# Optimization experiments

Measured on AMD Instinct MI355X. Metric: run time of the kernel, lower is better.

## Reference

```python
import jax, jax.numpy as jnp
import numpy as np

HIDDEN = 1024
NUM_EXPERTS = 8
TOP_K = 2
INNER = HIDDEN * 2
B, S = 4, 2048


def setup_inputs() -> dict:
    key = jax.random.key(0)
    ks = jax.random.split(key, 8)
    sd = 1.0 / np.sqrt(HIDDEN)
    si = 1.0 / np.sqrt(INNER)
    return {
        "x": jax.random.normal(ks[0], (B, S, HIDDEN), dtype=jnp.float32),
        "Wr": jax.random.uniform(ks[1], (HIDDEN, NUM_EXPERTS), jnp.float32, -sd, sd),
        "br": jax.random.uniform(ks[2], (NUM_EXPERTS,), jnp.float32, -sd, sd),
        "W1": jax.random.uniform(ks[3], (NUM_EXPERTS, HIDDEN, INNER), jnp.float32, -sd, sd),
        "b1": jax.random.uniform(ks[4], (NUM_EXPERTS, INNER), jnp.float32, -sd, sd),
        "W2": jax.random.uniform(ks[5], (NUM_EXPERTS, INNER, HIDDEN), jnp.float32, -si, si),
        "b2": jax.random.uniform(ks[6], (NUM_EXPERTS, HIDDEN), jnp.float32, -si, si),
    }


def reference(x, Wr, br, W1, b1, W2, b2):
    batch, seq, hidden = x.shape
    tokens = x.reshape(-1, hidden)                       # [N, d]
    n = tokens.shape[0]
    logits = tokens @ Wr + br                            # [N, E]
    top_w, top_i = jax.lax.top_k(logits, TOP_K)          # [N, k]
    top_w = jax.nn.softmax(top_w, axis=-1)
    # Dense per-token expert weights (zero outside top-k) — equivalent to the
    # sorted-dispatch + index_add combine in the original.
    weights = jnp.zeros((n, NUM_EXPERTS), dtype=top_w.dtype)
    weights = weights.at[jnp.arange(n)[:, None], top_i].add(top_w)  # [N, E]
    out = jnp.zeros_like(tokens)
    for e in range(NUM_EXPERTS):  # fixed small loop over experts
        h = jax.nn.relu(tokens @ W1[e] + b1[e])          # [N, inner]
        y = h @ W2[e] + b2[e]                            # [N, d]
        out = out + y * weights[:, e:e + 1]
    return out.reshape(batch, seq, hidden)
```

## Files before the change

### kernel.cpp

```cpp
#include <hip/hip_runtime.h>
#include <stdint.h>

#define HID    1024
#define EXPERTS 8
#define TOPK   2
#define INNER  2048
#define NTOK   8192
#define NPAIR  (NTOK * TOPK)
#define MAXT   136
#define BM 128
#define BN 256
#define BK 64
#define NSLOT 304
#define AFFS  24

typedef _Float16 f16;
typedef f16   f16x8 __attribute__((ext_vector_type(8)));
typedef float f32x4 __attribute__((ext_vector_type(4)));

#define VMCNT(n) asm volatile("s_waitcnt vmcnt(" #n ")" ::: "memory")
#define BARRIER() do { __builtin_amdgcn_s_barrier(); asm volatile("" ::: "memory"); } while (0)

__device__ __forceinline__ void gload_lds16(const void* g, void* l) {
  __builtin_amdgcn_global_load_lds(
      (const __attribute__((address_space(1))) void*)g,
      (__attribute__((address_space(3))) void*)l, 16, 0, 0);
}

__global__ void router_kernel(const float* __restrict__ x,
                              const float* __restrict__ Wr,
                              const float* __restrict__ br,
                              int* __restrict__ e_sel, float* __restrict__ w_sel) {
  int gid  = blockIdx.x * blockDim.x + threadIdx.x;
  int wid  = gid >> 6;
  int lane = gid & 63;
  if (wid >= NTOK) return;

  const f32x4* xr = (const f32x4*)(x + (size_t)wid * HID);
  float acc[EXPERTS];
#pragma unroll
  for (int e = 0; e < EXPERTS; ++e) acc[e] = 0.f;
#pragma unroll
  for (int j = 0; j < HID / 256; ++j) {
    f32x4 xv = xr[j * 64 + lane];
    int   k  = (j * 64 + lane) * 4;
    const float* wr = Wr + (size_t)k * EXPERTS;
#pragma unroll
    for (int r = 0; r < 4; ++r) {
      float xs = xv[r];
      f32x4 w0 = *(const f32x4*)(wr + r * 8);
      f32x4 w1 = *(const f32x4*)(wr + r * 8 + 4);
#pragma unroll
      for (int e = 0; e < 4; ++e) { acc[e] += xs * w0[e]; acc[4 + e] += xs * w1[e]; }
    }
  }
#pragma unroll
  for (int e = 0; e < EXPERTS; ++e) {
#pragma unroll
    for (int off = 32; off > 0; off >>= 1) acc[e] += __shfl_xor(acc[e], off);
  }
  if (lane == 0) {
    float lg[EXPERTS];
#pragma unroll
    for (int e = 0; e < EXPERTS; ++e) lg[e] = acc[e] + br[e];
    int e0 = 0; float l0 = lg[0];
#pragma unroll
    for (int e = 1; e < EXPERTS; ++e) if (lg[e] > l0) { l0 = lg[e]; e0 = e; }
    int e1 = -1; float l1 = -3.4e38f;
#pragma unroll
    for (int e = 0; e < EXPERTS; ++e) if (e != e0 && lg[e] > l1) { l1 = lg[e]; e1 = e; }
    float a  = __expf(l1 - l0);
    float w0 = 1.f / (1.f + a);
    float w1 = a * w0;
    e_sel[wid * 2]     = e0;  e_sel[wid * 2 + 1] = e1;
    w_sel[wid * 2]     = w0;  w_sel[wid * 2 + 1] = w1;
  }
}

__global__ __launch_bounds__(1024) void dispatch_kernel(
    const int* __restrict__ e_sel, const float* __restrict__ w_sel,
    int* __restrict__ tok_list, float* __restrict__ wt_list,
    int* __restrict__ counts, int* __restrict__ bases,
    int* __restrict__ slot_e, int* __restrict__ slot_m0,
    int* __restrict__ slot_g, int* __restrict__ tinfo) {
  __shared__ int scnt[EXPERTS][1024];
  __shared__ int etot[EXPERTS];
  __shared__ int ebase[EXPERTS];
  int tid = threadIdx.x, lane = tid & 63, wv = tid >> 6;

  int myE[16]; float myW[16];
  int lc[EXPERTS];
#pragma unroll
  for (int e = 0; e < EXPERTS; ++e) lc[e] = 0;
#pragma unroll
  for (int i = 0; i < 16; ++i) {
    int p = tid * 16 + i;
    myE[i] = e_sel[p];
    myW[i] = w_sel[p];
#pragma unroll
    for (int e = 0; e < EXPERTS; ++e) lc[e] += (myE[i] == e);
  }
#pragma unroll
  for (int e = 0; e < EXPERTS; ++e) scnt[e][tid] = lc[e];
  __syncthreads();

  if (wv < EXPERTS) {
    int run = 0;
    for (int c = 0; c < 16; ++c) {
      int v = scnt[wv][c * 64 + lane];
      int incl = v;
#pragma unroll
      for (int off = 1; off < 64; off <<= 1) {
        int n = __shfl_up(incl, off);
        if (lane >= off) incl += n;
      }
      scnt[wv][c * 64 + lane] = run + incl - v;
      run += __shfl(incl, 63);
    }
    if (lane == 0) etot[wv] = run;
  }
  __syncthreads();

  if (tid < NSLOT) slot_e[tid] = -1;
  __syncthreads();
  if (tid == 0) {
    int s = 0;
    for (int e = 0; e < EXPERTS; ++e) {
      ebase[e] = s; bases[e] = s; counts[e] = etot[e]; s += etot[e];
    }
    int ov = AFFS * EXPERTS, gt = 0;
    for (int e = 0; e < EXPERTS; ++e) {
      int ntl = (etot[e] + BM - 1) / BM;
      for (int i = 0; i < ntl; ++i) {
        int sl = (i < AFFS) ? (e + EXPERTS * i) : (ov++);
        slot_e[sl] = e; slot_m0[sl] = i * BM; slot_g[sl] = gt++;
      }
    }
    tinfo[0] = gt;
  }
  __syncthreads();

  int cur[EXPERTS];
#pragma unroll
  for (int e = 0; e < EXPERTS; ++e) cur[e] = ebase[e] + scnt[e][tid];
#pragma unroll
  for (int i = 0; i < 16; ++i) {
    int p = 0;
#pragma unroll
    for (int e = 0; e < EXPERTS; ++e) if (myE[i] == e) p = cur[e]++;
    tok_list[p] = (tid * 16 + i) >> 1;
    wt_list[p]  = myW[i];
  }
}

__global__ void convert_x_kernel(const float* __restrict__ x,
                                 f16* __restrict__ x16, int n8) {
  int i = blockIdx.x * blockDim.x + threadIdx.x;
  int stride = gridDim.x * blockDim.x;
  for (; i < n8; i += stride) {
    f32x4 a = ((const f32x4*)x)[i * 2];
    f32x4 b = ((const f32x4*)x)[i * 2 + 1];
    f16x8 o;
#pragma unroll
    for (int j = 0; j < 4; ++j) { o[j] = (f16)a[j]; o[4 + j] = (f16)b[j]; }
    ((f16x8*)x16)[i] = o;
  }
}

__global__ void transpose_cvt_kernel(const float* __restrict__ src,
                                     f16* __restrict__ dst, int R, int C) {
  __shared__ float tile[32][33];
  int z = blockIdx.z;
  src += (size_t)z * R * C;
  dst += (size_t)z * R * C;
  int c0 = blockIdx.x * 32, r0 = blockIdx.y * 32;
  int tx = threadIdx.x, ty = threadIdx.y;
#pragma unroll
  for (int i = 0; i < 4; ++i)
    tile[ty + i * 8][tx] = src[(size_t)(r0 + ty + i * 8) * C + c0 + tx];
  __syncthreads();
#pragma unroll
  for (int i = 0; i < 4; ++i)
    dst[(size_t)(c0 + ty + i * 8) * R + r0 + tx] = (f16)tile[tx][ty + i * 8];
}


#define STAGE6(BUF) do {                                                      \
  _Pragma("unroll") for (int i_ = 0; i_ < 2; ++i_) {                          \
    gload_lds16(gA[i_], (BUF) + i_ * 4096 + wid * 512); gA[i_] += BK;         \
  }                                                                           \
  _Pragma("unroll") for (int i_ = 0; i_ < 4; ++i_) {                          \
    gload_lds16(gB[i_], (BUF) + 8192 + i_ * 4096 + wid * 512); gB[i_] += BK;  \
  }                                                                           \
} while (0)

#define COMPUTE16(BUF) do {                                                   \
  _Pragma("unroll") for (int kk_ = 0; kk_ < 2; ++kk_) {                       \
    int lc_ = (kk_ * 4 + hi) ^ sa;                                            \
    f16x8 af_[4], bf_[4];                                                     \
    _Pragma("unroll") for (int mi_ = 0; mi_ < 4; ++mi_)                       \
      af_[mi_] = *(const f16x8*)((BUF) + (wm + mi_ * 16 + ar) * 64 + lc_ * 8);\
    _Pragma("unroll") for (int ni_ = 0; ni_ < 4; ++ni_)                       \
      bf_[ni_] = *(const f16x8*)((BUF) + 8192 +                               \
                                 (wn + ni_ * 16 + ar) * 64 + lc_ * 8);        \
    _Pragma("unroll") for (int mi_ = 0; mi_ < 4; ++mi_)                       \
      _Pragma("unroll") for (int ni_ = 0; ni_ < 4; ++ni_)                     \
        acc[mi_][ni_] = __builtin_amdgcn_mfma_f32_16x16x32_f16(               \
            af_[mi_], bf_[ni_], acc[mi_][ni_], 0, 0, 0);                      \
  }                                                                           \
} while (0)

#define PIPELINE_LOOP(NT) do {                                                \
  STAGE6(q0); STAGE6(q1);                                                     \
  VMCNT(6); BARRIER();                                                        \
  for (int t = 0; t < (NT); ++t) {                                            \
    if (t + 2 < (NT)) { STAGE6(q2); }                                         \
    COMPUTE16(q0);                                                            \
    if (t + 2 < (NT)) { VMCNT(6); } else { VMCNT(0); }                        \
    BARRIER();                                                                \
    f16* tm_ = q0; q0 = q1; q1 = q2; q2 = tm_;                                \
  }                                                                           \
} while (0)

__global__ __launch_bounds__(512, 2) void gemm1_kernel(
    const f16* __restrict__ x16, const f16* __restrict__ w1t,
    const float* __restrict__ bias1, const int* __restrict__ tok_list,
    const int* __restrict__ counts, const int* __restrict__ bases,
    const int* __restrict__ slot_e, const int* __restrict__ slot_m0,
    const int* __restrict__ slot_g, int c0, int G,
    f16* __restrict__ h16) {
  int sx = blockIdx.x;
  int e  = slot_e[sx];
  if (e < 0) return;
  int g  = slot_g[sx];
  if (g < c0 || g >= c0 + G) return;
  int m0 = slot_m0[sx];
  int cnt = counts[e], base = bases[e];
  int n0 = blockIdx.y * BN;
  const f16* Bg = w1t + (size_t)e * INNER * HID;

  __shared__ __align__(16) f16 LDS[3 * 24576];
  f16 *q0 = LDS, *q1 = LDS + 24576, *q2 = LDS + 2 * 24576;

  int tid = threadIdx.x, lane = tid & 63, wid = tid >> 6;
  int wm = (wid >> 2) * 64, wn = (wid & 3) * 64;
  int ar = lane & 15, hi = lane >> 4, sa = ar & 7;

  int trow = tid >> 3;
  int gcol = (tid & 7) ^ (trow & 7);
  const f16* gA[2];
  const f16* gB[4];
#pragma unroll
  for (int i = 0; i < 2; ++i) {
    int row = i * 64 + trow;
    int tok = tok_list[base + min(m0 + row, cnt - 1)];
    gA[i] = x16 + (size_t)tok * HID + gcol * 8;
  }
#pragma unroll
  for (int i = 0; i < 4; ++i) {
    int row = i * 64 + trow;
    gB[i] = Bg + (size_t)(n0 + row) * HID + gcol * 8;
  }

  f32x4 acc[4][4];
#pragma unroll
  for (int i = 0; i < 4; ++i)
#pragma unroll
    for (int j = 0; j < 4; ++j) acc[i][j] = (f32x4){0.f, 0.f, 0.f, 0.f};

  PIPELINE_LOOP(HID / BK);

  int colc = ar, rbase = hi * 4;
  float bb[4];
#pragma unroll
  for (int ni = 0; ni < 4; ++ni)
    bb[ni] = bias1[(size_t)e * INNER + n0 + wn + ni * 16 + colc];
#pragma unroll
  for (int mi = 0; mi < 4; ++mi)
#pragma unroll
    for (int r = 0; r < 4; ++r) {
      int ml = wm + mi * 16 + rbase + r;
      if (m0 + ml < cnt) {
        size_t rowoff = (size_t)((g - c0) * BM + ml) * INNER + n0 + wn + colc;
#pragma unroll
        for (int ni = 0; ni < 4; ++ni) {
          float v = acc[mi][ni][r] + bb[ni];
          h16[rowoff + ni * 16] = (f16)fmaxf(v, 0.f);
        }
      }
    }
}

__global__ __launch_bounds__(512, 2) void gemm2_kernel(
    const f16* __restrict__ h16, const f16* __restrict__ w2t,
    const float* __restrict__ bias2, const int* __restrict__ tok_list,
    const float* __restrict__ wt_list, const int* __restrict__ counts,
    const int* __restrict__ bases,
    const int* __restrict__ slot_e, const int* __restrict__ slot_m0,
    const int* __restrict__ slot_g, int c0, int G,
    float* __restrict__ out) {
  int sx = blockIdx.x;
  int e  = slot_e[sx];
  if (e < 0) return;
  int g  = slot_g[sx];
  if (g < c0 || g >= c0 + G) return;
  int m0 = slot_m0[sx];
  int cnt = counts[e], base = bases[e];
  int d0 = blockIdx.y * BN;
  int kc = blockIdx.z;
  int koff = kc * (INNER / 2);
  const f16* Bg = w2t + (size_t)e * HID * INNER;

  __shared__ __align__(16) f16 LDS[3 * 24576];
  f16 *q0 = LDS, *q1 = LDS + 24576, *q2 = LDS + 2 * 24576;

  int tid = threadIdx.x, lane = tid & 63, wid = tid >> 6;
  int wm = (wid >> 2) * 64, wn = (wid & 3) * 64;
  int ar = lane & 15, hi = lane >> 4, sa = ar & 7;

  int trow = tid >> 3;
  int gcol = (tid & 7) ^ (trow & 7);
  const f16* gA[2];
  const f16* gB[4];
#pragma unroll
  for (int i = 0; i < 2; ++i) {
    int row  = i * 64 + trow;
    int lrow = min(m0 + row, cnt - 1) - m0;
    gA[i] = h16 + ((size_t)(g - c0) * BM + lrow) * INNER + koff + gcol * 8;
  }
#pragma unroll
  for (int i = 0; i < 4; ++i) {
    int row = i * 64 + trow;
    gB[i] = Bg + (size_t)(d0 + row) * INNER + koff + gcol * 8;
  }

  f32x4 acc[4][4];
#pragma unroll
  for (int i = 0; i < 4; ++i)
#pragma unroll
    for (int j = 0; j < 4; ++j) acc[i][j] = (f32x4){0.f, 0.f, 0.f, 0.f};

  PIPELINE_LOOP((INNER / 2) / BK);

  int colc = ar, rbase = hi * 4;
  float bb[4];
#pragma unroll
  for (int ni = 0; ni < 4; ++ni)
    bb[ni] = (kc == 0) ? bias2[(size_t)e * HID + d0 + wn + ni * 16 + colc] : 0.f;
#pragma unroll
  for (int mi = 0; mi < 4; ++mi)
#pragma unroll
    for (int r = 0; r < 4; ++r) {
      int ml = wm + mi * 16 + rbase + r;
      if (m0 + ml < cnt) {
        int   p   = base + m0 + ml;
        int   tok = tok_list[p];
        float w   = wt_list[p];
        float* orow = out + (size_t)tok * HID + d0 + wn + colc;
#pragma unroll
        for (int ni = 0; ni < 4; ++ni) {
          float v = acc[mi][ni][r] + bb[ni];
          atomicAdd(orow + ni * 16, v * w);
        }
      }
    }
}

extern "C" void kernel_launch(void* const* d_in, const int* in_sizes, int n_in,
                              void* d_out, int out_size, void* d_ws, size_t ws_size,
                              hipStream_t stream) {
  (void)in_sizes; (void)n_in;
  const float* x  = (const float*)d_in[0];
  const float* Wr = (const float*)d_in[1];
  const float* br = (const float*)d_in[2];
  const float* W1 = (const float*)d_in[3];
  const float* b1 = (const float*)d_in[4];
  const float* W2 = (const float*)d_in[5];
  const float* b2 = (const float*)d_in[6];
  float* out = (float*)d_out;

  char*  ws  = (char*)d_ws;
  size_t off = 0;
  auto alloc = [&](size_t bytes) {
    char* p = ws + off;
    off += bytes; off = (off + 255) & ~(size_t)255;
    return p;
  };
  int*   tok_list = (int*)alloc(NPAIR * sizeof(int));
  float* wt_list  = (float*)alloc(NPAIR * sizeof(float));
  int*   e_sel    = (int*)alloc(NTOK * 2 * sizeof(int));
  float* w_sel    = (float*)alloc(NTOK * 2 * sizeof(float));
  int*   counts   = (int*)alloc(EXPERTS * sizeof(int));
  int*   bases    = (int*)alloc(EXPERTS * sizeof(int));
  int*   slot_e   = (int*)alloc(NSLOT * sizeof(int));
  int*   slot_m0  = (int*)alloc(NSLOT * sizeof(int));
  int*   slot_g   = (int*)alloc(NSLOT * sizeof(int));
  int*   tinfo    = (int*)alloc(16 * sizeof(int));
  f16*   w1t      = (f16*)alloc((size_t)EXPERTS * HID * INNER * sizeof(f16));
  f16*   w2t      = (f16*)alloc((size_t)EXPERTS * HID * INNER * sizeof(f16));
  f16*   x16      = (f16*)alloc((size_t)NTOK * HID * sizeof(f16));
  const size_t TILE_BYTES = (size_t)BM * INNER * sizeof(f16);
  size_t rem = (ws_size > off) ? (ws_size - off) : 0;
  int G = (int)(rem / TILE_BYTES);
  if (G < 1) G = 1;
  if (G > MAXT) G = MAXT;
  int nch = (MAXT + G - 1) / G;
  f16* h16 = (f16*)(ws + off);

  hipMemsetAsync(out, 0, (size_t)out_size * sizeof(float), stream);

  convert_x_kernel<<<2048, 256, 0, stream>>>(x, x16, NTOK * HID / 8);
  transpose_cvt_kernel<<<dim3(INNER / 32, HID / 32, EXPERTS), dim3(32, 8), 0, stream>>>(
      W1, w1t, HID, INNER);
  transpose_cvt_kernel<<<dim3(HID / 32, INNER / 32, EXPERTS), dim3(32, 8), 0, stream>>>(
      W2, w2t, INNER, HID);
  router_kernel<<<NTOK / 4, 256, 0, stream>>>(x, Wr, br, e_sel, w_sel);
  dispatch_kernel<<<1, 1024, 0, stream>>>(e_sel, w_sel, tok_list, wt_list,
                                          counts, bases, slot_e, slot_m0, slot_g, tinfo);

  for (int c = 0; c < nch; ++c) {
    int c0 = c * G;
    gemm1_kernel<<<dim3(NSLOT, INNER / BN, 1), 512, 0, stream>>>(
        x16, w1t, b1, tok_list, counts, bases, slot_e, slot_m0, slot_g, c0, G, h16);
    gemm2_kernel<<<dim3(NSLOT, HID / BN, 2), 512, 0, stream>>>(
        h16, w2t, b2, tok_list, wt_list, counts, bases, slot_e, slot_m0, slot_g, c0, G, out);
  }
}
```

Baseline: 533.4 us.

## Shrink GEMM tiles to 128x128x32 with 256-thread blocks and new swizzle

Both expert GEMM kernels now use 128x128 output tiles with BK=32 and 4 waves per block instead of 128x256 tiles, BK=64 and 8 waves. The LDS staging layout and XOR swizzle are rewritten for 32-wide rows, and launch bounds and the slot/affinity constants are changed to match. The aim is a smaller LDS footprint, more resident blocks per CU and more blocks to fill the GPU. In exchange each block reuses loaded data less, and the shorter K step means more barriers per unit of work.

```diff
diff --git a/kernel.cpp b/kernel.cpp
--- a/kernel.cpp
+++ b/kernel.cpp
@@ -9,10 +9,10 @@
 #define NPAIR  (NTOK * TOPK)
 #define MAXT   136
 #define BM 128
-#define BN 256
-#define BK 64
-#define NSLOT 304
-#define AFFS  24
+#define BN 128
+#define BK 32
+#define AFFS  17
+#define NSLOT 200
 
 typedef _Float16 f16;
 typedef f16   f16x8 __attribute__((ext_vector_type(8)));
@@ -185,44 +185,39 @@
 }
 
 
-#define STAGE6(BUF) do {                                                      \
+#define STAGE4(BUF) do {                                                      \
   _Pragma("unroll") for (int i_ = 0; i_ < 2; ++i_) {                          \
-    gload_lds16(gA[i_], (BUF) + i_ * 4096 + wid * 512); gA[i_] += BK;         \
-  }                                                                           \
-  _Pragma("unroll") for (int i_ = 0; i_ < 4; ++i_) {                          \
-    gload_lds16(gB[i_], (BUF) + 8192 + i_ * 4096 + wid * 512); gB[i_] += BK;  \
+    gload_lds16(gA[i_], (BUF) + i_ * 2048 + wid * 512); gA[i_] += BK;         \
+    gload_lds16(gB[i_], (BUF) + 4096 + i_ * 2048 + wid * 512); gB[i_] += BK;  \
   }                                                                           \
 } while (0)
 
-#define COMPUTE16(BUF) do {                                                   \
-  _Pragma("unroll") for (int kk_ = 0; kk_ < 2; ++kk_) {                       \
-    int lc_ = (kk_ * 4 + hi) ^ sa;                                            \
-    f16x8 af_[4], bf_[4];                                                     \
-    _Pragma("unroll") for (int mi_ = 0; mi_ < 4; ++mi_)                       \
-      af_[mi_] = *(const f16x8*)((BUF) + (wm + mi_ * 16 + ar) * 64 + lc_ * 8);\
+#define COMPUTE8(BUF) do {                                                    \
+  f16x8 af_[4], bf_[4];                                                       \
+  _Pragma("unroll") for (int mi_ = 0; mi_ < 4; ++mi_)                         \
+    af_[mi_] = *(const f16x8*)((BUF) + (wm + mi_ * 16 + ar) * 32 + cswz * 8); \
+  _Pragma("unroll") for (int ni_ = 0; ni_ < 4; ++ni_)                         \
+    bf_[ni_] = *(const f16x8*)((BUF) + 4096 +                                 \
+                               (wn + ni_ * 16 + ar) * 32 + cswz * 8);         \
+  _Pragma("unroll") for (int mi_ = 0; mi_ < 4; ++mi_)                         \
     _Pragma("unroll") for (int ni_ = 0; ni_ < 4; ++ni_)                       \
-      bf_[ni_] = *(const f16x8*)((BUF) + 8192 +                               \
-                                 (wn + ni_ * 16 + ar) * 64 + lc_ * 8);        \
-    _Pragma("unroll") for (int mi_ = 0; mi_ < 4; ++mi_)                       \
-      _Pragma("unroll") for (int ni_ = 0; ni_ < 4; ++ni_)                     \
-        acc[mi_][ni_] = __builtin_amdgcn_mfma_f32_16x16x32_f16(               \
-            af_[mi_], bf_[ni_], acc[mi_][ni_], 0, 0, 0);                      \
-  }                                                                           \
+      acc[mi_][ni_] = __builtin_amdgcn_mfma_f32_16x16x32_f16(                 \
+          af_[mi_], bf_[ni_], acc[mi_][ni_], 0, 0, 0);                        \
 } while (0)
 
 #define PIPELINE_LOOP(NT) do {                                                \
-  STAGE6(q0); STAGE6(q1);                                                     \
-  VMCNT(6); BARRIER();                                                        \
+  STAGE4(q0); STAGE4(q1);                                                     \
+  VMCNT(4); BARRIER();                                                        \
   for (int t = 0; t < (NT); ++t) {                                            \
-    if (t + 2 < (NT)) { STAGE6(q2); }                                         \
-    COMPUTE16(q0);                                                            \
-    if (t + 2 < (NT)) { VMCNT(6); } else { VMCNT(0); }                        \
+    if (t + 2 < (NT)) { STAGE4(q2); }                                         \
+    COMPUTE8(q0);                                                             \
+    if (t + 2 < (NT)) { VMCNT(4); } else { VMCNT(0); }                        \
     BARRIER();                                                                \
     f16* tm_ = q0; q0 = q1; q1 = q2; q2 = tm_;                                \
   }                                                                           \
 } while (0)
 
-__global__ __launch_bounds__(512, 2) void gemm1_kernel(
+__global__ __launch_bounds__(256, 3) void gemm1_kernel(
     const f16* __restrict__ x16, const f16* __restrict__ w1t,
     const float* __restrict__ bias1, const int* __restrict__ tok_list,
     const int* __restrict__ counts, const int* __restrict__ bases,
@@ -239,26 +234,23 @@
   int n0 = blockIdx.y * BN;
   const f16* Bg = w1t + (size_t)e * INNER * HID;
 
-  __shared__ __align__(16) f16 LDS[3 * 24576];
-  f16 *q0 = LDS, *q1 = LDS + 24576, *q2 = LDS + 2 * 24576;
+  __shared__ __align__(16) f16 LDS[3 * 8192];
+  f16 *q0 = LDS, *q1 = LDS + 8192, *q2 = LDS + 2 * 8192;
 
   int tid = threadIdx.x, lane = tid & 63, wid = tid >> 6;
-  int wm = (wid >> 2) * 64, wn = (wid & 3) * 64;
-  int ar = lane & 15, hi = lane >> 4, sa = ar & 7;
-
-  int trow = tid >> 3;
-  int gcol = (tid & 7) ^ (trow & 7);
+  int wm = (wid >> 1) * 64, wn = (wid & 1) * 64;
+  int ar = lane & 15, hi = lane >> 4;
+  int cswz = hi ^ ((ar >> 1) & 3);
+
+  int trow = tid >> 2;
+  int gcol = (tid & 3) ^ ((tid >> 3) & 3);
   const f16* gA[2];
-  const f16* gB[4];
+  const f16* gB[2];
 #pragma unroll
   for (int i = 0; i < 2; ++i) {
     int row = i * 64 + trow;
     int tok = tok_list[base + min(m0 + row, cnt - 1)];
     gA[i] = x16 + (size_t)tok * HID + gcol * 8;
-  }
-#pragma unroll
-  for (int i = 0; i < 4; ++i) {
-    int row = i * 64 + trow;
     gB[i] = Bg + (size_t)(n0 + row) * HID + gcol * 8;
   }
 
@@ -291,7 +283,7 @@
     }
 }
 
-__global__ __launch_bounds__(512, 2) void gemm2_kernel(
+__global__ __launch_bounds__(256, 3) void gemm2_kernel(
     const f16* __restrict__ h16, const f16* __restrict__ w2t,
     const float* __restrict__ bias2, const int* __restrict__ tok_list,
     const float* __restrict__ wt_list, const int* __restrict__ counts,
@@ -311,26 +303,23 @@
   int koff = kc * (INNER / 2);
   const f16* Bg = w2t + (size_t)e * HID * INNER;
 
-  __shared__ __align__(16) f16 LDS[3 * 24576];
-  f16 *q0 = LDS, *q1 = LDS + 24576, *q2 = LDS + 2 * 24576;
+  __shared__ __align__(16) f16 LDS[3 * 8192];
+  f16 *q0 = LDS, *q1 = LDS + 8192, *q2 = LDS + 2 * 8192;
 
   int tid = threadIdx.x, lane = tid & 63, wid = tid >> 6;
-  int wm = (wid >> 2) * 64, wn = (wid & 3) * 64;
-  int ar = lane & 15, hi = lane >> 4, sa = ar & 7;
-
-  int trow = tid >> 3;
-  int gcol = (tid & 7) ^ (trow & 7);
+  int wm = (wid >> 1) * 64, wn = (wid & 1) * 64;
+  int ar = lane & 15, hi = lane >> 4;
+  int cswz = hi ^ ((ar >> 1) & 3);
+
+  int trow = tid >> 2;
+  int gcol = (tid & 3) ^ ((tid >> 3) & 3);
   const f16* gA[2];
-  const f16* gB[4];
+  const f16* gB[2];
 #pragma unroll
   for (int i = 0; i < 2; ++i) {
     int row  = i * 64 + trow;
     int lrow = min(m0 + row, cnt - 1) - m0;
     gA[i] = h16 + ((size_t)(g - c0) * BM + lrow) * INNER + koff + gcol * 8;
-  }
-#pragma unroll
-  for (int i = 0; i < 4; ++i) {
-    int row = i * 64 + trow;
     gB[i] = Bg + (size_t)(d0 + row) * INNER + koff + gcol * 8;
   }
 
@@ -420,9 +409,9 @@
 
   for (int c = 0; c < nch; ++c) {
     int c0 = c * G;
-    gemm1_kernel<<<dim3(NSLOT, INNER / BN, 1), 512, 0, stream>>>(
+    gemm1_kernel<<<dim3(NSLOT, INNER / BN, 1), 256, 0, stream>>>(
         x16, w1t, b1, tok_list, counts, bases, slot_e, slot_m0, slot_g, c0, G, h16);
-    gemm2_kernel<<<dim3(NSLOT, HID / BN, 2), 512, 0, stream>>>(
+    gemm2_kernel<<<dim3(NSLOT, HID / BN, 2), 256, 0, stream>>>(
         h16, w2t, b2, tok_list, wt_list, counts, bases, slot_e, slot_m0, slot_g, c0, G, out);
   }
 }
```

Result: faster. 502.7 us (-5.8%).
